# Performance work log

Measured on AMD Instinct MI355X. Metric: run time of the kernel, lower is better.

Reference implementation:

```python
import jax, jax.numpy as jnp
import numpy as np

HID = 1024
HEADS = 16
HEAD_DIM = HID // HEADS
NEG = -10000000000.0


def setup_inputs() -> dict:
    key = jax.random.key(0)
    ks = jax.random.split(key, 12)
    B, S = 4, 2048
    scale = 1.0 / np.sqrt(HID)
    inp = {
        "query": jax.random.normal(ks[0], (B, S, HID), dtype=jnp.float32),
        "key": jax.random.normal(ks[1], (B, S, HID), dtype=jnp.float32),
        "value": jax.random.normal(ks[2], (B, S, HID), dtype=jnp.float32),
        "Wq": jax.random.normal(ks[3], (HID, HID), dtype=jnp.float32) * scale,
        "bq": jnp.zeros((HID,), dtype=jnp.float32),
        "Wk": jax.random.normal(ks[4], (HID, HID), dtype=jnp.float32) * scale,
        "bk": jnp.zeros((HID,), dtype=jnp.float32),
        "Wv": jax.random.normal(ks[5], (HID, HID), dtype=jnp.float32) * scale,
        "bv": jnp.zeros((HID,), dtype=jnp.float32),
        "Wo": jax.random.normal(ks[6], (HID, HID), dtype=jnp.float32) * scale,
        "bo": jnp.zeros((HID,), dtype=jnp.float32),
    }
    return inp


def reference(query, key, value, Wq, bq, Wk, bk, Wv, bv, Wo, bo):
    B, S, _ = query.shape
    # linear projections (nn.Linear: x @ W.T + b)
    q = query @ Wq.T + bq
    k = key @ Wk.T + bk
    v = value @ Wv.T + bv
    # split heads -> [B, H, S, D]
    q = q.reshape(B, S, HEADS, HEAD_DIM).transpose(0, 2, 1, 3)
    k = k.reshape(B, S, HEADS, HEAD_DIM).transpose(0, 2, 1, 3)
    v = v.reshape(B, S, HEADS, HEAD_DIM).transpose(0, 2, 1, 3)
    # NOTE: original module computes self.scale but never applies it -> unscaled logits
    attn = jnp.einsum("bhqd,bhkd->bhqk", q, k)
    causal = jnp.tril(jnp.ones((S, S), dtype=bool))
    attn = jnp.where(causal, attn, NEG)
    attn = jax.nn.softmax(attn, axis=-1)
    x = jnp.einsum("bhqk,bhkd->bhqd", attn, v)
    x = x.transpose(0, 2, 1, 3).reshape(B, S, HID)
    return x @ Wo.T + bo
```

## Files before the change

### kernel.cpp

```cpp
#include <hip/hip_runtime.h>
#include <hip/hip_fp16.h>

typedef _Float16 half_t;
typedef half_t halfx8 __attribute__((ext_vector_type(8)));
typedef half_t halfx4 __attribute__((ext_vector_type(4)));
typedef float floatx4 __attribute__((ext_vector_type(4)));

#define HID 1024
#define HEADS 16
#define HD 64
#define BATCH 4
#define SEQ 2048
#define MTOT (BATCH * SEQ)
#define NWELEM (HID * HID)

#define MFMA_F16 __builtin_amdgcn_mfma_f32_16x16x32_f16

#define VM_WAIT(n) asm volatile("s_waitcnt vmcnt(" #n ")" ::: "memory")
#define BARRIER()  asm volatile("s_barrier" ::: "memory")

__device__ inline halfx8 load8h(const half_t* p) { return *(const halfx8*)p; }
__device__ inline halfx8 load8h(const float* p) {
    floatx4 x = *(const floatx4*)p;
    floatx4 y = *(const floatx4*)(p + 4);
    halfx8 r;
    r[0] = (half_t)x[0]; r[1] = (half_t)x[1];
    r[2] = (half_t)x[2]; r[3] = (half_t)x[3];
    r[4] = (half_t)y[0]; r[5] = (half_t)y[1];
    r[6] = (half_t)y[2]; r[7] = (half_t)y[3];
    return r;
}

__device__ __forceinline__ uint32_t pack2h(float a, float b) {
    union { half_t h[2]; uint32_t u; } r;
    r.h[0] = (half_t)a; r.h[1] = (half_t)b;
    return r.u;
}

__device__ __forceinline__ void gl_lds16(const half_t* g, half_t* lds) {
    __builtin_amdgcn_global_load_lds(
        (const __attribute__((address_space(1))) void*)g,
        (__attribute__((address_space(3))) void*)lds, 16, 0, 0);
}

__device__ __forceinline__ void pl32swap(uint32_t& a, uint32_t& b) {
    asm volatile("v_permlane32_swap_b32 %0, %1" : "+v"(a), "+v"(b));
}
__device__ __forceinline__ void pl16swap(uint32_t& a, uint32_t& b) {
    asm volatile("v_permlane16_swap_b32 %0, %1" : "+v"(a), "+v"(b));
}
__device__ __forceinline__ float quad_max(float x) {
    uint32_t a = __builtin_bit_cast(uint32_t, x), b;
    asm volatile("v_mov_b32 %0, %1" : "=v"(b) : "v"(a));
    pl16swap(a, b);
    float m = fmaxf(__builtin_bit_cast(float, a), __builtin_bit_cast(float, b));
    uint32_t c = __builtin_bit_cast(uint32_t, m), d;
    asm volatile("v_mov_b32 %0, %1" : "=v"(d) : "v"(c));
    pl32swap(c, d);
    return fmaxf(__builtin_bit_cast(float, c), __builtin_bit_cast(float, d));
}
__device__ __forceinline__ float quad_sum(float x) {
    uint32_t a = __builtin_bit_cast(uint32_t, x), b;
    asm volatile("v_mov_b32 %0, %1" : "=v"(b) : "v"(a));
    pl16swap(a, b);
    float s = __builtin_bit_cast(float, a) + __builtin_bit_cast(float, b);
    uint32_t c = __builtin_bit_cast(uint32_t, s), d;
    asm volatile("v_mov_b32 %0, %1" : "=v"(d) : "v"(c));
    pl32swap(c, d);
    return __builtin_bit_cast(float, c) + __builtin_bit_cast(float, d);
}

template <int MODE, typename TOut>
__device__ __forceinline__ void epilogue_store(
    const floatx4 (&acc)[4][4], const float* __restrict__ bias,
    TOut* __restrict__ Out, int m0, int n0, int wm, int wn, int quad, int l16)
{
    float bvals[4];
#pragma unroll
    for (int nt = 0; nt < 4; ++nt)
        bvals[nt] = bias[n0 + wn + nt * 16 + l16];

#pragma unroll
    for (int mt = 0; mt < 4; ++mt) {
        const int mbase = m0 + wm + mt * 16 + quad * 4;
#pragma unroll
        for (int nt = 0; nt < 4; ++nt) {
            const int n = n0 + wn + nt * 16 + l16;
            if (MODE == 2) {
                const int b = mbase >> 11, s = mbase & (SEQ - 1);
                const int h = n >> 6, d = n & (HD - 1);
                halfx4 st;
#pragma unroll
                for (int r = 0; r < 4; ++r)
                    st[r] = (half_t)(acc[mt][nt][r] + bvals[nt]);
                *(halfx4*)((half_t*)Out +
                    ((((size_t)b * HEADS + h) * HD + d) << 11) + s) = st;
            } else {
#pragma unroll
                for (int r = 0; r < 4; ++r) {
                    const float v = acc[mt][nt][r] + bvals[nt];
                    const int mm  = mbase + r;
                    if (MODE == 0) {
                        const int b = mm >> 11, s = mm & (SEQ - 1);
                        const int h = n >> 6, d = n & (HD - 1);
                        Out[((((size_t)b * HEADS + h) * SEQ + s) << 6) + d] = (TOut)v;
                    } else {
                        Out[(size_t)mm * HID + n] = (TOut)v;
                    }
                }
            }
        }
    }
}

template <int MODE, typename TOut>
__global__ __launch_bounds__(256) void gemm16(
    const half_t* __restrict__ A, const half_t* __restrict__ W,
    const float* __restrict__ bias, TOut* __restrict__ Out)
{
    __shared__ half_t As[4][128 * 32];
    __shared__ half_t Bs[4][128 * 32];

    const int tid  = threadIdx.x;
    const int id   = blockIdx.y * gridDim.x + blockIdx.x;
    const int cpx  = (gridDim.x * gridDim.y) >> 3;
    const int swz  = (id & 7) * cpx + (id >> 3);
    const int m0   = (swz >> 3) * 128;
    const int n0   = (swz & 7) * 128;
    const int wave = tid >> 6;
    const int lane = tid & 63;
    const int quad = lane >> 4;
    const int l16  = lane & 15;
    const int wm   = (wave >> 1) * 64;
    const int wn   = (wave & 1) * 64;

    const int c0   = wave * 2;
    const int srow = c0 * 16 + (lane >> 2);
    const int scol = (lane & 3) * 8;
    const half_t* aptr0 = A + (size_t)(m0 + srow) * HID + scol;
    const half_t* aptr1 = aptr0 + (size_t)16 * HID;
    const half_t* bptr0 = W + (size_t)(n0 + srow) * HID + scol;
    const half_t* bptr1 = bptr0 + (size_t)16 * HID;

    floatx4 acc[4][4];
    const floatx4 zero4 = {0.f, 0.f, 0.f, 0.f};
#pragma unroll
    for (int mt = 0; mt < 4; ++mt)
#pragma unroll
        for (int nt = 0; nt < 4; ++nt) acc[mt][nt] = zero4;

    auto stage = [&](int buf, int k0) {
        gl_lds16(aptr0 + k0, &As[buf][c0 * 512]);
        gl_lds16(aptr1 + k0, &As[buf][c0 * 512 + 512]);
        gl_lds16(bptr0 + k0, &Bs[buf][c0 * 512]);
        gl_lds16(bptr1 + k0, &Bs[buf][c0 * 512 + 512]);
    };
    auto compute = [&](int buf) {
        halfx8 af[4], bfr[4];
#pragma unroll
        for (int t = 0; t < 4; ++t) {
            af[t]  = *(const halfx8*)&As[buf][(wm + t * 16 + l16) * 32 + quad * 8];
            bfr[t] = *(const halfx8*)&Bs[buf][(wn + t * 16 + l16) * 32 + quad * 8];
        }
#pragma unroll
        for (int mt = 0; mt < 4; ++mt)
#pragma unroll
            for (int nt = 0; nt < 4; ++nt)
                acc[mt][nt] = MFMA_F16(af[mt], bfr[nt], acc[mt][nt], 0, 0, 0);
    };

    stage(0, 0);
    stage(1, 32);
    stage(2, 64);
    for (int t = 0; t < 32; ++t) {
        if (t < 30)       VM_WAIT(8);
        else if (t == 30) VM_WAIT(4);
        else              VM_WAIT(0);
        BARRIER();
        if (t < 29) stage((t + 3) & 3, (t + 3) * 32);
        compute(t & 3);
    }

    epilogue_store<MODE, TOut>(acc, bias, Out, m0, n0, wm, wn, quad, l16);
}

template <int MODE, typename TA, typename TOut>
__global__ __launch_bounds__(256) void gemm_bt(
    const TA* __restrict__ A, const float* __restrict__ W,
    const float* __restrict__ bias, TOut* __restrict__ Out)
{
    __shared__ half_t As[128][40];
    __shared__ half_t Bs[128][40];

    const int tid  = threadIdx.x;
    const int m0   = blockIdx.y * 128;
    const int n0   = blockIdx.x * 128;
    const int wave = tid >> 6;
    const int lane = tid & 63;
    const int quad = lane >> 4;
    const int l16  = lane & 15;
    const int wm   = (wave >> 1) * 64;
    const int wn   = (wave & 1) * 64;
    const int trow = tid >> 1;
    const int tcol = (tid & 1) * 16;

    const TA*    aptr = A + (size_t)(m0 + trow) * HID + tcol;
    const float* bptr = W + (size_t)(n0 + trow) * HID + tcol;

    floatx4 acc[4][4];
    const floatx4 zero4 = {0.f, 0.f, 0.f, 0.f};
#pragma unroll
    for (int mt = 0; mt < 4; ++mt)
#pragma unroll
        for (int nt = 0; nt < 4; ++nt) acc[mt][nt] = zero4;

    for (int k0 = 0; k0 < HID; k0 += 32) {
        halfx8 av0 = load8h(aptr);
        halfx8 av1 = load8h(aptr + 8);
        halfx8 bv0 = load8h(bptr);
        halfx8 bv1 = load8h(bptr + 8);
        aptr += 32;
        bptr += 32;

        __syncthreads();
        *(halfx8*)&As[trow][tcol]     = av0;
        *(halfx8*)&As[trow][tcol + 8] = av1;
        *(halfx8*)&Bs[trow][tcol]     = bv0;
        *(halfx8*)&Bs[trow][tcol + 8] = bv1;
        __syncthreads();

        halfx8 af[4], bfr[4];
#pragma unroll
        for (int t = 0; t < 4; ++t) {
            af[t]  = *(const halfx8*)&As[wm + t * 16 + l16][quad * 8];
            bfr[t] = *(const halfx8*)&Bs[wn + t * 16 + l16][quad * 8];
        }
#pragma unroll
        for (int mt = 0; mt < 4; ++mt)
#pragma unroll
            for (int nt = 0; nt < 4; ++nt)
                acc[mt][nt] = MFMA_F16(af[mt], bfr[nt], acc[mt][nt], 0, 0, 0);
    }

    epilogue_store<MODE, TOut>(acc, bias, Out, m0, n0, wm, wn, quad, l16);
}

__global__ __launch_bounds__(256) void cvt_act3(
    const float* __restrict__ q, const float* __restrict__ k,
    const float* __restrict__ v,
    half_t* __restrict__ q16, half_t* __restrict__ k16, half_t* __restrict__ v16)
{
    const int t = blockIdx.y;
    const float* src = (t == 0) ? q : (t == 1) ? k : v;
    half_t* dst = (t == 0) ? q16 : (t == 1) ? k16 : v16;
    const size_t i = ((size_t)blockIdx.x * 256 + threadIdx.x) * 8;
    *(halfx8*)(dst + i) = load8h(src + i);
}

__global__ __launch_bounds__(256) void cvt_w4(
    const float* __restrict__ w0, const float* __restrict__ w1,
    const float* __restrict__ w2, const float* __restrict__ w3,
    half_t* __restrict__ out)
{
    const int t = blockIdx.y;
    const float* src = (t == 0) ? w0 : (t == 1) ? w1 : (t == 2) ? w2 : w3;
    const size_t i = ((size_t)blockIdx.x * 256 + threadIdx.x) * 8;
    *(halfx8*)(out + (size_t)t * NWELEM + i) = load8h(src + i);
}

__global__ __launch_bounds__(256) void attn_kernel(
    const half_t* __restrict__ Q, const half_t* __restrict__ K,
    const half_t* __restrict__ VT, half_t* __restrict__ O)
{
    __shared__ half_t Ks[64][72];
    __shared__ half_t Vt[64][72];

    const int bh  = blockIdx.x;
    const int qt  = (gridDim.y - 1) - blockIdx.y;
    const int q0  = qt * 128;
    const int tid = threadIdx.x;
    const int wave = tid >> 6;
    const int lane = tid & 63;
    const int quad = lane >> 4;
    const int l16  = lane & 15;

    const half_t* Qb  = Q  + (size_t)bh * SEQ * HD;
    const half_t* Kb  = K  + (size_t)bh * SEQ * HD;
    const half_t* VTb = VT + (size_t)bh * HD * SEQ;

    halfx8 aq[2][2];
#pragma unroll
    for (int mt = 0; mt < 2; ++mt) {
        const half_t* p = Qb + (size_t)(q0 + wave * 32 + mt * 16 + l16) * HD + quad * 8;
        aq[mt][0] = *(const halfx8*)p;
        aq[mt][1] = *(const halfx8*)(p + 32);
    }

    const floatx4 zero4 = {0.f, 0.f, 0.f, 0.f};
    floatx4 oaccT[2][4];
    float mrow[2], lrow[2];
#pragma unroll
    for (int mt = 0; mt < 2; ++mt) {
        mrow[mt] = -3.0e38f;
        lrow[mt] = 0.f;
#pragma unroll
        for (int dt = 0; dt < 4; ++dt) oaccT[mt][dt] = zero4;
    }

    const int srow = tid >> 2;
    const int scol = (tid & 3) * 16;
    const int ktiles = 2 * qt + 2;

    union U8 { halfx8 h; uint32_t u[4]; };

    halfx8 nk0, nk1, nv0, nv1;
    {
        const half_t* ksrc = Kb + (size_t)srow * HD + scol;
        nk0 = *(const halfx8*)ksrc;
        nk1 = *(const halfx8*)(ksrc + 8);
        const half_t* vsrc = VTb + (size_t)srow * SEQ + scol;
        nv0 = *(const halfx8*)vsrc;
        nv1 = *(const halfx8*)(vsrc + 8);
    }

    for (int kt = 0; kt < ktiles; ++kt) {
        const int k0 = kt * 64;
        __syncthreads();
        *(halfx8*)&Ks[srow][scol]     = nk0;
        *(halfx8*)&Ks[srow][scol + 8] = nk1;
        *(halfx8*)&Vt[srow][scol]     = nv0;
        *(halfx8*)&Vt[srow][scol + 8] = nv1;
        __syncthreads();

        if (kt + 1 < ktiles) {
            const int kn = k0 + 64;
            const half_t* ksrc = Kb + (size_t)(kn + srow) * HD + scol;
            nk0 = *(const halfx8*)ksrc;
            nk1 = *(const halfx8*)(ksrc + 8);
            const half_t* vsrc = VTb + (size_t)srow * SEQ + kn + scol;
            nv0 = *(const halfx8*)vsrc;
            nv1 = *(const halfx8*)(vsrc + 8);
        }

        const bool active = (k0 <= q0 + wave * 32 + 31);

        if (active) {
            floatx4 sacc[2][4];
#pragma unroll
            for (int mt = 0; mt < 2; ++mt)
#pragma unroll
                for (int nt = 0; nt < 4; ++nt) sacc[mt][nt] = zero4;
#pragma unroll
            for (int nt = 0; nt < 4; ++nt) {
                halfx8 bk0 = *(const halfx8*)&Ks[nt * 16 + l16][quad * 8];
                halfx8 bk1 = *(const halfx8*)&Ks[nt * 16 + l16][quad * 8 + 32];
#pragma unroll
                for (int mt = 0; mt < 2; ++mt) {
                    sacc[mt][nt] = MFMA_F16(bk0, aq[mt][0], sacc[mt][nt], 0, 0, 0);
                    sacc[mt][nt] = MFMA_F16(bk1, aq[mt][1], sacc[mt][nt], 0, 0, 0);
                }
            }

            if (kt >= 2 * qt) {
#pragma unroll
                for (int mt = 0; mt < 2; ++mt) {
                    const int qg = q0 + wave * 32 + mt * 16 + l16;
#pragma unroll
                    for (int nt = 0; nt < 4; ++nt) {
                        const int kg = k0 + nt * 16 + quad * 4;
#pragma unroll
                        for (int r = 0; r < 4; ++r)
                            if (kg + r > qg) sacc[mt][nt][r] = -1.0e30f;
                    }
                }
            }

            uint32_t pk[2][4][2];
#pragma unroll
            for (int mt = 0; mt < 2; ++mt) {
                float mx = sacc[mt][0][0];
#pragma unroll
                for (int nt = 0; nt < 4; ++nt)
#pragma unroll
                    for (int r = 0; r < 4; ++r)
                        if (nt | r) mx = fmaxf(mx, sacc[mt][nt][r]);
                mx = quad_max(mx);

                if (!__all(mx <= mrow[mt] + 8.f)) {
                    const float mnew  = fmaxf(mrow[mt], mx);
                    const float alpha = __expf(mrow[mt] - mnew);
                    mrow[mt] = mnew;
                    lrow[mt] *= alpha;
#pragma unroll
                    for (int dt = 0; dt < 4; ++dt) oaccT[mt][dt] *= alpha;
                }

                float rsum = 0.f;
#pragma unroll
                for (int nt = 0; nt < 4; ++nt)
#pragma unroll
                    for (int r = 0; r < 4; ++r) {
                        const float p = __expf(sacc[mt][nt][r] - mrow[mt]);
                        sacc[mt][nt][r] = p;
                        rsum += p;
                    }
#pragma unroll
                for (int nt = 0; nt < 4; ++nt) {
                    pk[mt][nt][0] = pack2h(sacc[mt][nt][0], sacc[mt][nt][1]);
                    pk[mt][nt][1] = pack2h(sacc[mt][nt][2], sacc[mt][nt][3]);
                }
                lrow[mt] += quad_sum(rsum);
            }

            U8 pb[2][2];
#pragma unroll
            for (int mt = 0; mt < 2; ++mt)
#pragma unroll
                for (int s2 = 0; s2 < 2; ++s2)
#pragma unroll
                    for (int h = 0; h < 2; ++h) {
                        uint32_t a = pk[mt][2 * s2][h];
                        uint32_t b = pk[mt][2 * s2 + 1][h];
                        pl32swap(a, b);
                        pl16swap(a, b);
                        pb[mt][s2].u[h]     = a;
                        pb[mt][s2].u[2 + h] = b;
                    }

#pragma unroll
            for (int s2 = 0; s2 < 2; ++s2)
#pragma unroll
                for (int dt = 0; dt < 4; ++dt) {
                    halfx8 bv = *(const halfx8*)&Vt[dt * 16 + l16][s2 * 32 + quad * 8];
                    oaccT[0][dt] = MFMA_F16(bv, pb[0][s2].h, oaccT[0][dt], 0, 0, 0);
                    oaccT[1][dt] = MFMA_F16(bv, pb[1][s2].h, oaccT[1][dt], 0, 0, 0);
                }
        }
    }

    const int b = bh >> 4, h = bh & (HEADS - 1);
#pragma unroll
    for (int mt = 0; mt < 2; ++mt) {
        const int q = q0 + wave * 32 + mt * 16 + l16;
#pragma unroll
        for (int dt = 0; dt < 4; ++dt) {
            halfx4 st;
#pragma unroll
            for (int r = 0; r < 4; ++r)
                st[r] = (half_t)(oaccT[mt][dt][r] / lrow[mt]);
            *(halfx4*)(O + (size_t)(b * SEQ + q) * HID +
                       h * HD + dt * 16 + quad * 4) = st;
        }
    }
}

extern "C" void kernel_launch(void* const* d_in, const int* in_sizes, int n_in,
                              void* d_out, int out_size, void* d_ws, size_t ws_size,
                              hipStream_t stream)
{
    const float* query = (const float*)d_in[0];
    const float* key   = (const float*)d_in[1];
    const float* value = (const float*)d_in[2];
    const float* Wq    = (const float*)d_in[3];
    const float* bq    = (const float*)d_in[4];
    const float* Wk    = (const float*)d_in[5];
    const float* bk    = (const float*)d_in[6];
    const float* Wv    = (const float*)d_in[7];
    const float* bv    = (const float*)d_in[8];
    const float* Wo    = (const float*)d_in[9];
    const float* bo    = (const float*)d_in[10];
    float* out = (float*)d_out;

    const size_t NE = (size_t)MTOT * HID;
    half_t* Qp  = (half_t*)d_ws;
    half_t* Kp  = Qp  + NE;
    half_t* VpT = Kp  + NE;
    half_t* Ob  = VpT + NE;
    half_t* W16 = Ob  + NE;
    const size_t need = (4 * NE + 4 * (size_t)NWELEM) * sizeof(half_t);

    dim3 gg(HID / 128, MTOT / 128);
    dim3 ga(BATCH * HEADS, SEQ / 128);

    if (ws_size >= need && (size_t)out_size >= 2 * NE * sizeof(half_t)) {
        half_t* q16 = (half_t*)out;
        half_t* k16 = q16 + NE;
        half_t* v16 = Ob;
        const unsigned actBlocks = (unsigned)(NE / 2048);
        const unsigned wBlocks   = (unsigned)(NWELEM / 2048);

        cvt_w4<<<dim3(wBlocks, 4), 256, 0, stream>>>(Wq, Wk, Wv, Wo, W16);
        cvt_act3<<<dim3(actBlocks, 3), 256, 0, stream>>>(
            query, key, value, q16, k16, v16);

        gemm16<0, half_t><<<gg, 256, 0, stream>>>(q16, W16, bq, Qp);
        gemm16<0, half_t><<<gg, 256, 0, stream>>>(k16, W16 + NWELEM, bk, Kp);
        gemm16<2, half_t><<<gg, 256, 0, stream>>>(v16, W16 + 2 * (size_t)NWELEM, bv, VpT);

        attn_kernel<<<ga, 256, 0, stream>>>(Qp, Kp, VpT, Ob);

        gemm16<1, float><<<gg, 256, 0, stream>>>(Ob, W16 + 3 * (size_t)NWELEM, bo, out);
    } else {
        gemm_bt<0, float, half_t><<<gg, 256, 0, stream>>>(query, Wq, bq, Qp);
        gemm_bt<0, float, half_t><<<gg, 256, 0, stream>>>(key,   Wk, bk, Kp);
        gemm_bt<2, float, half_t><<<gg, 256, 0, stream>>>(value, Wv, bv, VpT);
        attn_kernel<<<ga, 256, 0, stream>>>(Qp, Kp, VpT, Ob);
        gemm_bt<1, half_t, float><<<gg, 256, 0, stream>>>(Ob, Wo, bo, out);
    }
}
```

Baseline: 419.7 us.

## Shrink fp16 GEMM tile to 128x64 with double-buffered LDS pipeline

Halves the N dimension of the gemm16 tile from 128 to 64, so each wave computes a 64x32 block and the grid doubles to 1024 blocks. The 4-stage async pipeline with explicit vmcnt waits is replaced by a simpler 2-buffer loop synchronised with __syncthreads. LDS use drops and more blocks can run per CU, at the cost of less data reuse per tile, more global traffic, and a shallower prefetch depth. The fallback gemm_bt path keeps the 128x128 grid and gets its own inlined epilogue.

```diff
diff --git a/kernel.cpp b/kernel.cpp
--- a/kernel.cpp
+++ b/kernel.cpp
@@ -15,9 +15,6 @@
 #define NWELEM (HID * HID)
 
 #define MFMA_F16 __builtin_amdgcn_mfma_f32_16x16x32_f16
-
-#define VM_WAIT(n) asm volatile("s_waitcnt vmcnt(" #n ")" ::: "memory")
-#define BARRIER()  asm volatile("s_barrier" ::: "memory")
 
 __device__ inline halfx8 load8h(const half_t* p) { return *(const halfx8*)p; }
 __device__ inline halfx8 load8h(const float* p) {
@@ -71,20 +68,20 @@
 }
 
 template <int MODE, typename TOut>
-__device__ __forceinline__ void epilogue_store(
-    const floatx4 (&acc)[4][4], const float* __restrict__ bias,
+__device__ __forceinline__ void epilogue_store42(
+    const floatx4 (&acc)[4][2], const float* __restrict__ bias,
     TOut* __restrict__ Out, int m0, int n0, int wm, int wn, int quad, int l16)
 {
-    float bvals[4];
-#pragma unroll
-    for (int nt = 0; nt < 4; ++nt)
+    float bvals[2];
+#pragma unroll
+    for (int nt = 0; nt < 2; ++nt)
         bvals[nt] = bias[n0 + wn + nt * 16 + l16];
 
 #pragma unroll
     for (int mt = 0; mt < 4; ++mt) {
         const int mbase = m0 + wm + mt * 16 + quad * 4;
 #pragma unroll
-        for (int nt = 0; nt < 4; ++nt) {
+        for (int nt = 0; nt < 2; ++nt) {
             const int n = n0 + wn + nt * 16 + l16;
             if (MODE == 2) {
                 const int b = mbase >> 11, s = mbase & (SEQ - 1);
@@ -118,70 +115,69 @@
     const half_t* __restrict__ A, const half_t* __restrict__ W,
     const float* __restrict__ bias, TOut* __restrict__ Out)
 {
-    __shared__ half_t As[4][128 * 32];
-    __shared__ half_t Bs[4][128 * 32];
+    __shared__ half_t As[2][128 * 32];
+    __shared__ half_t Bs[2][64 * 32];
 
     const int tid  = threadIdx.x;
     const int id   = blockIdx.y * gridDim.x + blockIdx.x;
     const int cpx  = (gridDim.x * gridDim.y) >> 3;
     const int swz  = (id & 7) * cpx + (id >> 3);
-    const int m0   = (swz >> 3) * 128;
-    const int n0   = (swz & 7) * 128;
+    const int m0   = (swz >> 4) * 128;
+    const int n0   = (swz & 15) * 64;
     const int wave = tid >> 6;
     const int lane = tid & 63;
     const int quad = lane >> 4;
     const int l16  = lane & 15;
     const int wm   = (wave >> 1) * 64;
-    const int wn   = (wave & 1) * 64;
+    const int wn   = (wave & 1) * 32;
 
     const int c0   = wave * 2;
-    const int srow = c0 * 16 + (lane >> 2);
+    const int arow = c0 * 16 + (lane >> 2);
     const int scol = (lane & 3) * 8;
-    const half_t* aptr0 = A + (size_t)(m0 + srow) * HID + scol;
+    const half_t* aptr0 = A + (size_t)(m0 + arow) * HID + scol;
     const half_t* aptr1 = aptr0 + (size_t)16 * HID;
-    const half_t* bptr0 = W + (size_t)(n0 + srow) * HID + scol;
-    const half_t* bptr1 = bptr0 + (size_t)16 * HID;
-
-    floatx4 acc[4][4];
+    const int brow = wave * 16 + (lane >> 2);
+    const half_t* bptr0 = W + (size_t)(n0 + brow) * HID + scol;
+
+    floatx4 acc[4][2];
     const floatx4 zero4 = {0.f, 0.f, 0.f, 0.f};
 #pragma unroll
     for (int mt = 0; mt < 4; ++mt)
 #pragma unroll
-        for (int nt = 0; nt < 4; ++nt) acc[mt][nt] = zero4;
+        for (int nt = 0; nt < 2; ++nt) acc[mt][nt] = zero4;
 
     auto stage = [&](int buf, int k0) {
         gl_lds16(aptr0 + k0, &As[buf][c0 * 512]);
         gl_lds16(aptr1 + k0, &As[buf][c0 * 512 + 512]);
-        gl_lds16(bptr0 + k0, &Bs[buf][c0 * 512]);
-        gl_lds16(bptr1 + k0, &Bs[buf][c0 * 512 + 512]);
+        gl_lds16(bptr0 + k0, &Bs[buf][wave * 512]);
     };
     auto compute = [&](int buf) {
-        halfx8 af[4], bfr[4];
-#pragma unroll
-        for (int t = 0; t < 4; ++t) {
+        halfx8 af[4], bfr[2];
+#pragma unroll
+        for (int t = 0; t < 4; ++t)
             af[t]  = *(const halfx8*)&As[buf][(wm + t * 16 + l16) * 32 + quad * 8];
+#pragma unroll
+        for (int t = 0; t < 2; ++t)
             bfr[t] = *(const halfx8*)&Bs[buf][(wn + t * 16 + l16) * 32 + quad * 8];
-        }
 #pragma unroll
         for (int mt = 0; mt < 4; ++mt)
 #pragma unroll
-            for (int nt = 0; nt < 4; ++nt)
+            for (int nt = 0; nt < 2; ++nt)
                 acc[mt][nt] = MFMA_F16(af[mt], bfr[nt], acc[mt][nt], 0, 0, 0);
     };
 
     stage(0, 0);
-    stage(1, 32);
-    stage(2, 64);
-    for (int t = 0; t < 32; ++t) {
-        if (t < 30)       VM_WAIT(8);
-        else if (t == 30) VM_WAIT(4);
-        else              VM_WAIT(0);
-        BARRIER();
-        if (t < 29) stage((t + 3) & 3, (t + 3) * 32);
-        compute(t & 3);
-    }
-
-    epilogue_store<MODE, TOut>(acc, bias, Out, m0, n0, wm, wn, quad, l16);
+    __syncthreads();
+    for (int k0 = 0; k0 < HID; k0 += 64) {
+        stage(1, k0 + 32);
+        compute(0);
+        __syncthreads();
+        if (k0 + 64 < HID) stage(0, k0 + 64);
+        compute(1);
+        __syncthreads();
+    }
+
+    epilogue_store42<MODE, TOut>(acc, bias, Out, m0, n0, wm, wn, quad, l16);
 }
 
 template <int MODE, typename TA, typename TOut>
@@ -242,7 +238,41 @@
                 acc[mt][nt] = MFMA_F16(af[mt], bfr[nt], acc[mt][nt], 0, 0, 0);
     }
 
-    epilogue_store<MODE, TOut>(acc, bias, Out, m0, n0, wm, wn, quad, l16);
+    float bvals[4];
+#pragma unroll
+    for (int nt = 0; nt < 4; ++nt)
+        bvals[nt] = bias[n0 + wn + nt * 16 + l16];
+#pragma unroll
+    for (int mt = 0; mt < 4; ++mt) {
+        const int mbase = m0 + wm + mt * 16 + quad * 4;
+#pragma unroll
+        for (int nt = 0; nt < 4; ++nt) {
+            const int n = n0 + wn + nt * 16 + l16;
+            if (MODE == 2) {
+                const int b = mbase >> 11, s = mbase & (SEQ - 1);
+                const int h = n >> 6, d = n & (HD - 1);
+                halfx4 st;
+#pragma unroll
+                for (int r = 0; r < 4; ++r)
+                    st[r] = (half_t)(acc[mt][nt][r] + bvals[nt]);
+                *(halfx4*)((half_t*)Out +
+                    ((((size_t)b * HEADS + h) * HD + d) << 11) + s) = st;
+            } else {
+#pragma unroll
+                for (int r = 0; r < 4; ++r) {
+                    const float v = acc[mt][nt][r] + bvals[nt];
+                    const int mm  = mbase + r;
+                    if (MODE == 0) {
+                        const int b = mm >> 11, s = mm & (SEQ - 1);
+                        const int h = n >> 6, d = n & (HD - 1);
+                        Out[((((size_t)b * HEADS + h) * SEQ + s) << 6) + d] = (TOut)v;
+                    } else {
+                        Out[(size_t)mm * HID + n] = (TOut)v;
+                    }
+                }
+            }
+        }
+    }
 }
 
 __global__ __launch_bounds__(256) void cvt_act3(
@@ -479,7 +509,8 @@
     half_t* W16 = Ob  + NE;
     const size_t need = (4 * NE + 4 * (size_t)NWELEM) * sizeof(half_t);
 
-    dim3 gg(HID / 128, MTOT / 128);
+    dim3 gg(HID / 64, MTOT / 128);
+    dim3 ggL(HID / 128, MTOT / 128);
     dim3 ga(BATCH * HEADS, SEQ / 128);
 
     if (ws_size >= need && (size_t)out_size >= 2 * NE * sizeof(half_t)) {
@@ -501,10 +532,10 @@
 
         gemm16<1, float><<<gg, 256, 0, stream>>>(Ob, W16 + 3 * (size_t)NWELEM, bo, out);
     } else {
-        gemm_bt<0, float, half_t><<<gg, 256, 0, stream>>>(query, Wq, bq, Qp);
-        gemm_bt<0, float, half_t><<<gg, 256, 0, stream>>>(key,   Wk, bk, Kp);
-        gemm_bt<2, float, half_t><<<gg, 256, 0, stream>>>(value, Wv, bv, VpT);
+        gemm_bt<0, float, half_t><<<ggL, 256, 0, stream>>>(query, Wq, bq, Qp);
+        gemm_bt<0, float, half_t><<<ggL, 256, 0, stream>>>(key,   Wk, bk, Kp);
+        gemm_bt<2, float, half_t><<<ggL, 256, 0, stream>>>(value, Wv, bv, VpT);
         attn_kernel<<<ga, 256, 0, stream>>>(Qp, Kp, VpT, Ob);
-        gemm_bt<1, half_t, float><<<gg, 256, 0, stream>>>(Ob, Wo, bo, out);
-    }
-}
+        gemm_bt<1, half_t, float><<<ggL, 256, 0, stream>>>(Ob, Wo, bo, out);
+    }
+}
```

New measurement: 419.5 us. Within noise of the previous version (-0.0%).
